# Optimization experiments

Hardware: AMD Instinct MI355X
Metric: run time of the kernel (lower is better)

The kernel has to match this reference:

```python
import jax, jax.numpy as jnp
import numpy as np

B, C, N, H = 8, 256, 2048, 4
DIM = C // H
EPS = 1e-5
SLOPE = 0.2


def conv1x1(W, b, x):
    # W: [out, in], x: [B, in, N] -> [B, out, N]
    return jnp.einsum('oc,bcn->bon', W, x) + b[None, :, None]


def setup_inputs() -> dict:
    key = jax.random.key(0)
    ks = jax.random.split(key, 16)
    s = 1.0 / np.sqrt(C)
    s2 = 1.0 / np.sqrt(2 * C)
    return {
        'init_query': jax.random.normal(ks[0], (B, C, N), jnp.float32),
        'key': jax.random.normal(ks[1], (B, C, N), jnp.float32),
        'value': jax.random.normal(ks[2], (B, C, N), jnp.float32),
        'Wq': jax.random.normal(ks[3], (C, C), jnp.float32) * s,
        'bq': jax.random.normal(ks[4], (C,), jnp.float32) * s,
        'Wk': jax.random.normal(ks[5], (C, C), jnp.float32) * s,
        'bk': jax.random.normal(ks[6], (C,), jnp.float32) * s,
        'Wv': jax.random.normal(ks[7], (C, C), jnp.float32) * s,
        'bv': jax.random.normal(ks[8], (C,), jnp.float32) * s,
        'Wm': jax.random.normal(ks[9], (C, C), jnp.float32) * s,
        'bm': jax.random.normal(ks[10], (C,), jnp.float32) * s,
        'W1': jax.random.normal(ks[11], (2 * C, 2 * C), jnp.float32) * s2,
        'b1': jax.random.normal(ks[12], (2 * C,), jnp.float32) * s2,
        'gamma': jnp.ones((2 * C,), jnp.float32),
        'beta': jnp.zeros((2 * C,), jnp.float32),
        'W2': jax.random.normal(ks[13], (C, 2 * C), jnp.float32) * s2,
        'b2': jnp.zeros((C,), jnp.float32),  # nn.init.constant_(bias, 0.0)
    }


def reference(init_query, key, value, Wq, bq, Wk, bk, Wv, bv, Wm, bm, W1, b1, gamma, beta, W2, b2):
    # projections, then view [B, C, N] -> [B, dim, H, N] (dim outermost, matching torch .view)
    q = conv1x1(Wq, bq, init_query).reshape(B, DIM, H, N)
    k = conv1x1(Wk, bk, key).reshape(B, DIM, H, N)
    v = conv1x1(Wv, bv, value).reshape(B, DIM, H, N)
    scores = jnp.einsum('bdhn,bdhm->bhnm', q, k) / jnp.sqrt(jnp.float32(DIM))
    attn = jax.nn.softmax(scores, axis=-1)  # [B, H, N, N]
    x = jnp.einsum('bhnm,bdhm->bdhn', attn, v).reshape(B, C, N)
    x = conv1x1(Wm, bm, x)
    # post_merge: conv1x1 -> BatchNorm1d (training-mode batch stats) -> LeakyReLU(0.2) -> conv1x1
    h = conv1x1(W1, b1, jnp.concatenate([x, init_query], axis=1))  # [B, 2C, N]
    mu = jnp.mean(h, axis=(0, 2), keepdims=True)
    var = jnp.mean(jnp.square(h - mu), axis=(0, 2), keepdims=True)  # biased var, as torch BN
    hn = (h - mu) / jnp.sqrt(var + EPS) * gamma[None, :, None] + beta[None, :, None]
    hn = jnp.where(hn > 0, hn, SLOPE * hn)
    out = conv1x1(W2, b2, hn)
    return (out, attn)
```

## Files before the change

### kernel.cpp

```cpp
#include <hip/hip_runtime.h>
#include <stdint.h>

typedef __bf16 bf16x8 __attribute__((ext_vector_type(8)));
typedef float f32x4 __attribute__((ext_vector_type(4)));

constexpr int NB = 8;
constexpr int NC = 256;
constexpr int NN = 2048;
constexpr int NH = 4;
constexpr int ND = 64;
constexpr int NC2 = 512;
constexpr size_t TND = (size_t)NB * NN * NC;
__device__ constexpr float C2 = 0.125f * 1.4426950408889634f;

__device__ __forceinline__ ushort f2bf(float f) {
  union { float f; uint32_t u; } x; x.f = f;
  return (ushort)((x.u + 0x7FFFu + ((x.u >> 16) & 1u)) >> 16);
}
__device__ __forceinline__ float bf2f(ushort h) {
  union { uint32_t u; float f; } x; x.u = (uint32_t)h << 16;
  return x.f;
}


__global__ void k_cast(const float* __restrict__ s, ushort* __restrict__ d, int n) {
  int i = blockIdx.x * 256 + threadIdx.x;
  if (i < n) d[i] = f2bf(s[i]);
}

__global__ void k_cast3(const float* __restrict__ s0, const float* __restrict__ s1,
                        const float* __restrict__ s2, ushort* __restrict__ d) {
  int op = blockIdx.y;
  const float* s = op == 0 ? s0 : op == 1 ? s1 : s2;
  int i = blockIdx.x * 256 + threadIdx.x;
  d[(size_t)op * NC * NC + i] = f2bf(s[i]);
}

__global__ void k_cast_wm_perm(const float* __restrict__ s, ushort* __restrict__ d) {
  int i = blockIdx.x * 256 + threadIdx.x;
  int co = i >> 8, j = i & 255;
  int h = j >> 6, dd = j & 63;
  d[i] = f2bf(s[co * NC + dd * NH + h]);
}

__global__ void k_tc3(const float* __restrict__ s0, const float* __restrict__ s1,
                      const float* __restrict__ s2, ushort* __restrict__ d) {
  int n = blockIdx.x * 256 + threadIdx.x;
  int c0 = blockIdx.y * 8;
  int op = blockIdx.z >> 3, b = blockIdx.z & 7;
  const float* s = op == 0 ? s0 : op == 1 ? s1 : s2;
  const float* p = s + ((size_t)b * NC + c0) * NN + n;
  union { ushort u[8]; uint4 v; } t;
#pragma unroll
  for (int i = 0; i < 8; ++i) t.u[i] = f2bf(p[(size_t)i * NN]);
  *(uint4*)(d + (size_t)op * TND + ((size_t)b * NN + n) * NC + c0) = t.v;
}

__global__ void k_ht2(const ushort* __restrict__ s, ushort* __restrict__ d) {
  int n = blockIdx.x * 256 + threadIdx.x;
  int d0 = blockIdx.y * 8;
  int op = blockIdx.z >> 5, zz = blockIdx.z & 31, b = zz >> 2, h = zz & 3;
  const ushort* p = s + (size_t)op * TND + ((size_t)b * NC + (size_t)d0 * NH + h) * NN + n;
  union { ushort u[8]; uint4 v; } t;
#pragma unroll
  for (int i = 0; i < 8; ++i) t.u[i] = p[(size_t)i * NH * NN];
  *(uint4*)(d + (size_t)op * TND + ((size_t)zz * NN + n) * ND + d0) = t.v;
}

__global__ void k_bn_finalize(const float* __restrict__ stats, const float* __restrict__ gamma,
                              const float* __restrict__ beta, float4* __restrict__ aff) {
  int c = blockIdx.x * 256 + threadIdx.x;
  if (c >= NC2) return;
  const float inv_n = 1.f / (float)(NB * NN);
  float mu  = stats[c * 2] * inv_n;
  float var = stats[c * 2 + 1] * inv_n - mu * mu;
  float isg = gamma[c] * rsqrtf(var + 1e-5f);
  aff[c] = make_float4(mu, isg, beta[c], 0.f);
}


__device__ __forceinline__ bf16x8 ldtile(const ushort* base, int lr, int lg, int fc, int ks) {
  int row = fc * 16 + lr;
  int u = (ks * 4 + lg) ^ (lr & 7);
  return *(const bf16x8*)((const char*)base + row * 128 + u * 16);
}

__global__ __launch_bounds__(256, 4) void k_attn(
    const ushort* __restrict__ qt, const ushort* __restrict__ kt,
    const ushort* __restrict__ vnat, float* __restrict__ attn,
    ushort* __restrict__ xT) {
  __shared__ ushort Kl[2][4096];
  __shared__ ushort Vl[2][4096];
  __shared__ ushort Pl[4096];

  const int tid = threadIdx.x;
  const int lane = tid & 63, w = tid >> 6;
  const int lr = lane & 15, lg = lane >> 4;

  int flat = blockIdx.x;
  int xcd = flat & 7, idx = flat >> 3;
  int z = xcd * 4 + (idx >> 5);
  int r0 = (idx & 31) * 64;
  int b = z >> 2, h = z & 3;

  const ushort* kbase = kt + (size_t)z * NN * ND;
  const ushort* vbase = vnat + ((size_t)b * NC + h) * NN;

  const int sr0 = tid >> 3, sc0 = tid & 7;
  const int sr1 = 32 + sr0;
  const int d0 = sr0 * 128 + ((sc0 ^ (sr0 & 7)) << 4);
  const int d1 = sr1 * 128 + ((sc0 ^ (sr1 & 7)) << 4);

  bf16x8 aq0, aq1;
  {
    const ushort* qp = qt + ((size_t)z * NN + r0 + w * 16 + lr) * ND;
    aq0 = *(const bf16x8*)(qp + lg * 8);
    aq1 = *(const bf16x8*)(qp + 32 + lg * 8);
  }

  uint4 gk0, gk1, gv0, gv1;

  gk0 = *(const uint4*)(kbase + (size_t)sr0 * ND + sc0 * 8);
  gk1 = *(const uint4*)(kbase + (size_t)sr1 * ND + sc0 * 8);
  *(uint4*)((char*)Kl[0] + d0) = gk0;
  *(uint4*)((char*)Kl[0] + d1) = gk1;
  __syncthreads();

  float m_ln[4], s_ln[4];
#pragma unroll
  for (int j = 0; j < 4; ++j) { m_ln[j] = -INFINITY; s_ln[j] = 0.f; }

  for (int t = 0; t < 32; ++t) {
    int kb = t & 1;
    if (t < 31) {
      gk0 = *(const uint4*)(kbase + ((size_t)(t + 1) * 64 + sr0) * ND + sc0 * 8);
      gk1 = *(const uint4*)(kbase + ((size_t)(t + 1) * 64 + sr1) * ND + sc0 * 8);
    }
    f32x4 sa[4] = {};
#pragma unroll
    for (int ks = 0; ks < 2; ++ks) {
      bf16x8 aqk = ks ? aq1 : aq0;
#pragma unroll
      for (int fc = 0; fc < 4; ++fc)
        sa[fc] = __builtin_amdgcn_mfma_f32_16x16x32_bf16(aqk, ldtile(Kl[kb], lr, lg, fc, ks), sa[fc], 0, 0, 0);
    }
#pragma unroll
    for (int j = 0; j < 4; ++j) {
      float tm = fmaxf(fmaxf(sa[0][j], sa[1][j]), fmaxf(sa[2][j], sa[3][j]));
      float mn = fmaxf(m_ln[j], tm);
      float es = exp2f((sa[0][j] - mn) * C2) + exp2f((sa[1][j] - mn) * C2)
               + exp2f((sa[2][j] - mn) * C2) + exp2f((sa[3][j] - mn) * C2);
      s_ln[j] = s_ln[j] * exp2f((m_ln[j] - mn) * C2) + es;
      m_ln[j] = mn;
    }
    __syncthreads();
    if (t < 31) {
      *(uint4*)((char*)Kl[kb ^ 1] + d0) = gk0;
      *(uint4*)((char*)Kl[kb ^ 1] + d1) = gk1;
    }
    __syncthreads();
  }

  float m_run[4], inv_s[4];
#pragma unroll
  for (int j = 0; j < 4; ++j) {
    float m = m_ln[j];
#pragma unroll
    for (int o = 1; o < 16; o <<= 1) m = fmaxf(m, __shfl_xor(m, o));
    float c = s_ln[j] * exp2f((m_ln[j] - m) * C2);
#pragma unroll
    for (int o = 1; o < 16; o <<= 1) c += __shfl_xor(c, o);
    m_run[j] = m;
    inv_s[j] = 1.f / c;
  }

  gk0 = *(const uint4*)(kbase + (size_t)sr0 * ND + sc0 * 8);
  gk1 = *(const uint4*)(kbase + (size_t)sr1 * ND + sc0 * 8);
  gv0 = *(const uint4*)(vbase + (size_t)sr0 * 4 * NN + sc0 * 8);
  gv1 = *(const uint4*)(vbase + (size_t)sr1 * 4 * NN + sc0 * 8);
  *(uint4*)((char*)Kl[0] + d0) = gk0;
  *(uint4*)((char*)Kl[0] + d1) = gk1;
  *(uint4*)((char*)Vl[0] + d0) = gv0;
  *(uint4*)((char*)Vl[0] + d1) = gv1;
  __syncthreads();

  f32x4 acc[4] = {};
  const int prow = w * 16 + lr;
  char* plb = (char*)Pl;
  for (int t = 0; t < 32; ++t) {
    int kb = t & 1;
    if (t < 31) {
      gk0 = *(const uint4*)(kbase + ((size_t)(t + 1) * 64 + sr0) * ND + sc0 * 8);
      gk1 = *(const uint4*)(kbase + ((size_t)(t + 1) * 64 + sr1) * ND + sc0 * 8);
      gv0 = *(const uint4*)(vbase + (size_t)sr0 * 4 * NN + (t + 1) * 64 + sc0 * 8);
      gv1 = *(const uint4*)(vbase + (size_t)sr1 * 4 * NN + (t + 1) * 64 + sc0 * 8);
    }
    f32x4 sa[4] = {};
#pragma unroll
    for (int ks = 0; ks < 2; ++ks) {
      bf16x8 aqk = ks ? aq1 : aq0;
#pragma unroll
      for (int fc = 0; fc < 4; ++fc)
        sa[fc] = __builtin_amdgcn_mfma_f32_16x16x32_bf16(aqk, ldtile(Kl[kb], lr, lg, fc, ks), sa[fc], 0, 0, 0);
    }
#pragma unroll
    for (int fc = 0; fc < 4; ++fc)
#pragma unroll
      for (int j = 0; j < 4; ++j) {
        int row = w * 16 + lg * 4 + j;
        float p = exp2f((sa[fc][j] - m_run[j]) * C2) * inv_s[j];
        int byte = (row << 7) + ((fc * 16 + lr) << 1);
        byte ^= (row & 7) << 4;
        *(ushort*)(plb + byte) = f2bf(p);
      }
    float* abase = attn + ((size_t)z * NN + r0) * NN + t * 64;
#pragma unroll
    for (int k = 0; k < 4; ++k) {
      int row = w * 16 + lg + k * 4;
      int byte = (row << 7) + (lr << 3);
      byte ^= (row & 7) << 4;
      const ushort* pq = (const ushort*)(plb + byte);
      f32x4 vv = { bf2f(pq[0]), bf2f(pq[1]), bf2f(pq[2]), bf2f(pq[3]) };
      __builtin_nontemporal_store(vv, (f32x4*)(abase + (size_t)row * NN + lr * 4));
    }
#pragma unroll
    for (int ks = 0; ks < 2; ++ks) {
      int abyte = (prow << 7) + ks * 64 + lg * 16;
      abyte ^= (lr & 7) << 4;
      bf16x8 ap = *(const bf16x8*)(plb + abyte);
#pragma unroll
      for (int fc = 0; fc < 4; ++fc)
        acc[fc] = __builtin_amdgcn_mfma_f32_16x16x32_bf16(ap, ldtile(Vl[kb], lr, lg, fc, ks), acc[fc], 0, 0, 0);
    }
    __syncthreads();
    if (t < 31) {
      *(uint4*)((char*)Kl[kb ^ 1] + d0) = gk0;
      *(uint4*)((char*)Kl[kb ^ 1] + d1) = gk1;
      *(uint4*)((char*)Vl[kb ^ 1] + d0) = gv0;
      *(uint4*)((char*)Vl[kb ^ 1] + d1) = gv1;
    }
    __syncthreads();
  }
#pragma unroll
  for (int fc = 0; fc < 4; ++fc)
#pragma unroll
    for (int j = 0; j < 4; ++j) {
      int n = r0 + w * 16 + lg * 4 + j;
      xT[((size_t)b * NN + n) * NC + h * 64 + fc * 16 + lr] = f2bf(acc[fc][j]);
    }
}


enum GemmMode { M_PROJ = 0, M_WM, M_W1, M_W2 };

template <int MODE>
__global__ __launch_bounds__(256) void k_gemm(
    const ushort* __restrict__ A, const ushort* __restrict__ A2,
    const ushort* __restrict__ Bm,
    const float* __restrict__ bias, const float* __restrict__ bias_k,
    const float* __restrict__ bias_v, const float4* __restrict__ aff,
    float* __restrict__ stats, float* __restrict__ outf, ushort* __restrict__ outb) {
  constexpr int BR = (MODE == M_WM || MODE == M_W2) ? 64 : 128;
  constexpr int BC = 128;
  constexpr int KT = (MODE == M_PROJ || MODE == M_WM) ? 256 : 512;
  constexpr int FR = BR / 32;
  constexpr int FC = 4;
  constexpr int LDL = 72;

  __shared__ ushort ldsA[BR * LDL];
  __shared__ ushort ldsB[BC * LDL];

  const int tid = threadIdx.x;
  const int lane = tid & 63, wave = tid >> 6;
  const int wr = (wave >> 1) * (FR * 16), wc = (wave & 1) * (FC * 16);
  const int lr = lane & 15, lk = (lane >> 4) * 8;
  const int c0 = blockIdx.x * BC, r0 = blockIdx.y * BR;
  const int op = (MODE == M_PROJ) ? (int)(blockIdx.z >> 3) : 0;
  const size_t z = (MODE == M_PROJ) ? (blockIdx.z & 7) : blockIdx.z;

  f32x4 acc[FR][FC] = {};

  for (int kk = 0; kk < KT; kk += 64) {
    {
      const ushort* src; int ld;
      if constexpr (MODE == M_PROJ)        { src = A + (size_t)op * NC * NC + (size_t)r0 * NC + kk; ld = NC; }
      else if constexpr (MODE == M_WM)     { src = A + (z * NN + r0) * (size_t)NC + kk; ld = NC; }
      else if constexpr (MODE == M_W1) {
        if (kk < NC) src = A  + (z * NN + r0) * (size_t)NC + kk;
        else         src = A2 + (z * NN + r0) * (size_t)NC + (kk - NC);
        ld = NC;
      } else { src = A + (size_t)r0 * NC2 + kk; ld = NC2; }
#pragma unroll
      for (int i = 0; i < BR / 32; ++i) {
        int off = (tid + i * 256) * 8, row = off >> 6, k = off & 63;
        *(uint4*)&ldsA[row * LDL + k] = *(const uint4*)(src + (size_t)row * ld + k);
      }
    }
    if constexpr (MODE == M_W2) {
      const ushort* src = Bm + (z * NN + c0) * (size_t)NC2 + kk;
#pragma unroll
      for (int i = 0; i < BC / 32; ++i) {
        int off = (tid + i * 256) * 8, row = off >> 6, k = off & 63;
        union { ushort u[8]; uint4 v; } t, o;
        t.v = *(const uint4*)(src + (size_t)row * NC2 + k);
#pragma unroll
        for (int e = 0; e < 8; ++e) {
          float4 pr = aff[kk + k + e];
          float y = (bf2f(t.u[e]) - pr.x) * pr.y + pr.z;
          y = y > 0.f ? y : 0.2f * y;
          o.u[e] = f2bf(y);
        }
        *(uint4*)&ldsB[row * LDL + k] = o.v;
      }
    } else {
      const ushort* src; int ld;
      if constexpr (MODE == M_PROJ)        { src = Bm + (size_t)op * TND + (z * NN + c0) * (size_t)NC + kk; ld = NC; }
      else if constexpr (MODE == M_WM)     { src = Bm + (size_t)c0 * NC + kk; ld = NC; }
      else                                  { src = Bm + (size_t)c0 * NC2 + kk; ld = NC2; }
#pragma unroll
      for (int i = 0; i < BC / 32; ++i) {
        int off = (tid + i * 256) * 8, row = off >> 6, k = off & 63;
        *(uint4*)&ldsB[row * LDL + k] = *(const uint4*)(src + (size_t)row * ld + k);
      }
    }
    __syncthreads();
#pragma unroll
    for (int ks = 0; ks < 2; ++ks) {
      bf16x8 afr[FR], bfr[FC];
#pragma unroll
      for (int fr = 0; fr < FR; ++fr)
        afr[fr] = *(const bf16x8*)&ldsA[(wr + fr * 16 + lr) * LDL + ks * 32 + lk];
#pragma unroll
      for (int fc = 0; fc < FC; ++fc)
        bfr[fc] = *(const bf16x8*)&ldsB[(wc + fc * 16 + lr) * LDL + ks * 32 + lk];
#pragma unroll
      for (int fr = 0; fr < FR; ++fr)
#pragma unroll
        for (int fc = 0; fc < FC; ++fc)
          acc[fr][fc] = __builtin_amdgcn_mfma_f32_16x16x32_bf16(afr[fr], bfr[fc], acc[fr][fc], 0, 0, 0);
    }
    __syncthreads();
  }

  float sfc[FC], qfc[FC];
#pragma unroll
  for (int fc = 0; fc < FC; ++fc) { sfc[fc] = 0.f; qfc[fc] = 0.f; }
#pragma unroll
  for (int fr = 0; fr < FR; ++fr)
#pragma unroll
    for (int fc = 0; fc < FC; ++fc)
#pragma unroll
      for (int j = 0; j < 4; ++j) {
        int r = r0 + wr + fr * 16 + (lane >> 4) * 4 + j;
        int c = c0 + wc + fc * 16 + lr;
        float v = acc[fr][fc][j];
        if constexpr (MODE == M_PROJ) {
          const float* bb = op == 0 ? bias : op == 1 ? bias_k : bias_v;
          v += bb[r];
          outb[(size_t)op * TND + (z * NC + r) * (size_t)NN + c] = f2bf(v);
        } else if constexpr (MODE == M_WM) {
          v += bias[c];
          outb[(z * NN + r) * (size_t)NC + c] = f2bf(v);
        } else if constexpr (MODE == M_W1) {
          v += bias[c];
          outb[(z * NN + r) * (size_t)NC2 + c] = f2bf(v);
          sfc[fc] += v; qfc[fc] += v * v;
        } else {
          v += bias[r];
          outf[(z * NC + r) * (size_t)NN + c] = v;
        }
      }
  if constexpr (MODE == M_W1) {
#pragma unroll
    for (int fc = 0; fc < FC; ++fc) {
      float s1 = sfc[fc], s2 = qfc[fc];
      s1 += __shfl_xor(s1, 16); s1 += __shfl_xor(s1, 32);
      s2 += __shfl_xor(s2, 16); s2 += __shfl_xor(s2, 32);
      if (lane < 16) {
        int ch = c0 + wc + fc * 16 + lane;
        atomicAdd(&stats[ch * 2],     s1);
        atomicAdd(&stats[ch * 2 + 1], s2);
      }
    }
  }
}


extern "C" void kernel_launch(void* const* d_in, const int* in_sizes, int n_in,
                              void* d_out, int out_size, void* d_ws, size_t ws_size,
                              hipStream_t stream) {
  const float* iq    = (const float*)d_in[0];
  const float* keyi  = (const float*)d_in[1];
  const float* vali  = (const float*)d_in[2];
  const float* Wq = (const float*)d_in[3];  const float* bq = (const float*)d_in[4];
  const float* Wk = (const float*)d_in[5];  const float* bk = (const float*)d_in[6];
  const float* Wv = (const float*)d_in[7];  const float* bv = (const float*)d_in[8];
  const float* Wm = (const float*)d_in[9];  const float* bm = (const float*)d_in[10];
  const float* W1 = (const float*)d_in[11]; const float* b1 = (const float*)d_in[12];
  const float* gamma = (const float*)d_in[13]; const float* beta = (const float*)d_in[14];
  const float* W2 = (const float*)d_in[15]; const float* b2 = (const float*)d_in[16];

  float* out  = (float*)d_out;
  float* attn = out + (size_t)NB * NC * NN;

  uint8_t* cur = (uint8_t*)d_ws;
  auto alloc = [&](size_t bytes) { uint8_t* p = cur; cur += (bytes + 255) & ~(size_t)255; return p; };
  ushort* wq_b = (ushort*)alloc((size_t)NC * NC * 2 * 3);
  ushort* wm_b = (ushort*)alloc((size_t)NC * NC * 2);
  ushort* w1_b = (ushort*)alloc((size_t)NC2 * NC2 * 2);
  ushort* w2_b = (ushort*)alloc((size_t)NC * NC2 * 2);
  ushort* iqT   = (ushort*)alloc(TND * 2 * 3);
  ushort* q_nat = (ushort*)alloc(TND * 2 * 3);
  ushort* qt    = (ushort*)alloc(TND * 2 * 2);
  ushort* xT    = (ushort*)alloc(TND * 2);
  ushort* xmT   = (ushort*)alloc(TND * 2);
  ushort* hT    = (ushort*)alloc((size_t)NB * NN * NC2 * 2);
  float*  stats = (float*)alloc(NC2 * 2 * 4);
  float4* aff   = (float4*)alloc(NC2 * 16);
  ushort* kT    = iqT + TND;
  ushort* vT    = iqT + 2 * TND;
  ushort* v_nat = q_nat + 2 * TND;
  ushort* kt    = qt + TND;

  hipMemsetAsync(stats, 0, NC2 * 2 * 4, stream);

  k_cast3<<<dim3(256, 3), 256, 0, stream>>>(Wq, Wk, Wv, wq_b);
  k_cast_wm_perm<<<dim3(256), 256, 0, stream>>>(Wm, wm_b);
  k_cast<<<dim3(1024), 256, 0, stream>>>(W1, w1_b, NC2 * NC2);
  k_cast<<<dim3(512), 256, 0, stream>>>(W2, w2_b, NC * NC2);

  k_tc3<<<dim3(8, 32, 24), 256, 0, stream>>>(iq, keyi, vali, iqT);

  k_gemm<M_PROJ><<<dim3(16, 2, 24), 256, 0, stream>>>(wq_b, nullptr, iqT, bq, bk, bv, nullptr, nullptr, nullptr, q_nat);

  k_ht2<<<dim3(8, 8, 64), 256, 0, stream>>>(q_nat, qt);

  k_attn<<<dim3(1024), 256, 0, stream>>>(qt, kt, v_nat, attn, xT);

  k_gemm<M_WM><<<dim3(2, 32, 8), 256, 0, stream>>>(xT, nullptr, wm_b, bm, nullptr, nullptr, nullptr, nullptr, nullptr, xmT);

  k_gemm<M_W1><<<dim3(4, 16, 8), 256, 0, stream>>>(xmT, iqT, w1_b, b1, nullptr, nullptr, nullptr, stats, nullptr, hT);

  k_bn_finalize<<<dim3(2), 256, 0, stream>>>(stats, gamma, beta, aff);

  k_gemm<M_W2><<<dim3(16, 4, 8), 256, 0, stream>>>(w2_b, nullptr, hT, b2, nullptr, nullptr, aff, nullptr, out, nullptr);
}
```

Before: 290.6 us.

## Fuse input transpose-casts and head transpose into projection GEMM; pipeline attention loads

Removes the standalone fp32-to-bf16 transpose kernel and the head-transpose kernel. The projection GEMM now stages fp32 inputs directly into LDS and writes Q/K in per-head layout through an LDS transpose, with Wq/Wk rows permuted at cast time. The W1 GEMM reads init_query fp32 directly. Attention now prefetches K/V two tiles ahead, which drops one barrier per iteration. It also folds the softmax normalization into the exponent via log2 of the sum and stores fp32 probabilities straight to attn. These changes cut intermediate HBM traffic and kernel launches, at the cost of more complex GEMM staging and uncoalesced scalar attn stores.

After: 320.0 us. 1.1x slower.

```diff
diff --git a/kernel.cpp b/kernel.cpp
--- a/kernel.cpp
+++ b/kernel.cpp
@@ -28,12 +28,14 @@
   if (i < n) d[i] = f2bf(s[i]);
 }
 
-__global__ void k_cast3(const float* __restrict__ s0, const float* __restrict__ s1,
-                        const float* __restrict__ s2, ushort* __restrict__ d) {
+__global__ void k_cast_qkv(const float* __restrict__ s0, const float* __restrict__ s1,
+                           const float* __restrict__ s2, ushort* __restrict__ d) {
   int op = blockIdx.y;
   const float* s = op == 0 ? s0 : op == 1 ? s1 : s2;
   int i = blockIdx.x * 256 + threadIdx.x;
-  d[(size_t)op * NC * NC + i] = f2bf(s[i]);
+  int r = i >> 8, c = i & 255;
+  int orig = op < 2 ? (((r & 63) << 2) | (r >> 6)) : r;
+  d[(size_t)op * NC * NC + i] = f2bf(s[orig * NC + c]);
 }
 
 __global__ void k_cast_wm_perm(const float* __restrict__ s, ushort* __restrict__ d) {
@@ -41,30 +43,6 @@
   int co = i >> 8, j = i & 255;
   int h = j >> 6, dd = j & 63;
   d[i] = f2bf(s[co * NC + dd * NH + h]);
-}
-
-__global__ void k_tc3(const float* __restrict__ s0, const float* __restrict__ s1,
-                      const float* __restrict__ s2, ushort* __restrict__ d) {
-  int n = blockIdx.x * 256 + threadIdx.x;
-  int c0 = blockIdx.y * 8;
-  int op = blockIdx.z >> 3, b = blockIdx.z & 7;
-  const float* s = op == 0 ? s0 : op == 1 ? s1 : s2;
-  const float* p = s + ((size_t)b * NC + c0) * NN + n;
-  union { ushort u[8]; uint4 v; } t;
-#pragma unroll
-  for (int i = 0; i < 8; ++i) t.u[i] = f2bf(p[(size_t)i * NN]);
-  *(uint4*)(d + (size_t)op * TND + ((size_t)b * NN + n) * NC + c0) = t.v;
-}
-
-__global__ void k_ht2(const ushort* __restrict__ s, ushort* __restrict__ d) {
-  int n = blockIdx.x * 256 + threadIdx.x;
-  int d0 = blockIdx.y * 8;
-  int op = blockIdx.z >> 5, zz = blockIdx.z & 31, b = zz >> 2, h = zz & 3;
-  const ushort* p = s + (size_t)op * TND + ((size_t)b * NC + (size_t)d0 * NH + h) * NN + n;
-  union { ushort u[8]; uint4 v; } t;
-#pragma unroll
-  for (int i = 0; i < 8; ++i) t.u[i] = p[(size_t)i * NH * NN];
-  *(uint4*)(d + (size_t)op * TND + ((size_t)zz * NN + n) * ND + d0) = t.v;
 }
 
 __global__ void k_bn_finalize(const float* __restrict__ stats, const float* __restrict__ gamma,
@@ -124,6 +102,8 @@
   gk1 = *(const uint4*)(kbase + (size_t)sr1 * ND + sc0 * 8);
   *(uint4*)((char*)Kl[0] + d0) = gk0;
   *(uint4*)((char*)Kl[0] + d1) = gk1;
+  gk0 = *(const uint4*)(kbase + (size_t)(64 + sr0) * ND + sc0 * 8);
+  gk1 = *(const uint4*)(kbase + (size_t)(64 + sr1) * ND + sc0 * 8);
   __syncthreads();
 
   float m_ln[4], s_ln[4];
@@ -133,8 +113,12 @@
   for (int t = 0; t < 32; ++t) {
     int kb = t & 1;
     if (t < 31) {
-      gk0 = *(const uint4*)(kbase + ((size_t)(t + 1) * 64 + sr0) * ND + sc0 * 8);
-      gk1 = *(const uint4*)(kbase + ((size_t)(t + 1) * 64 + sr1) * ND + sc0 * 8);
+      *(uint4*)((char*)Kl[kb ^ 1] + d0) = gk0;
+      *(uint4*)((char*)Kl[kb ^ 1] + d1) = gk1;
+    }
+    if (t < 30) {
+      gk0 = *(const uint4*)(kbase + ((size_t)(t + 2) * 64 + sr0) * ND + sc0 * 8);
+      gk1 = *(const uint4*)(kbase + ((size_t)(t + 2) * 64 + sr1) * ND + sc0 * 8);
     }
     f32x4 sa[4] = {};
 #pragma unroll
@@ -148,20 +132,16 @@
     for (int j = 0; j < 4; ++j) {
       float tm = fmaxf(fmaxf(sa[0][j], sa[1][j]), fmaxf(sa[2][j], sa[3][j]));
       float mn = fmaxf(m_ln[j], tm);
-      float es = exp2f((sa[0][j] - mn) * C2) + exp2f((sa[1][j] - mn) * C2)
-               + exp2f((sa[2][j] - mn) * C2) + exp2f((sa[3][j] - mn) * C2);
-      s_ln[j] = s_ln[j] * exp2f((m_ln[j] - mn) * C2) + es;
+      float mnC = mn * C2;
+      float es = exp2f(fmaf(sa[0][j], C2, -mnC)) + exp2f(fmaf(sa[1][j], C2, -mnC))
+               + exp2f(fmaf(sa[2][j], C2, -mnC)) + exp2f(fmaf(sa[3][j], C2, -mnC));
+      s_ln[j] = s_ln[j] * exp2f(fmaf(m_ln[j], C2, -mnC)) + es;
       m_ln[j] = mn;
     }
     __syncthreads();
-    if (t < 31) {
-      *(uint4*)((char*)Kl[kb ^ 1] + d0) = gk0;
-      *(uint4*)((char*)Kl[kb ^ 1] + d1) = gk1;
-    }
-    __syncthreads();
-  }
-
-  float m_run[4], inv_s[4];
+  }
+
+  float mC[4];
 #pragma unroll
   for (int j = 0; j < 4; ++j) {
     float m = m_ln[j];
@@ -170,8 +150,7 @@
     float c = s_ln[j] * exp2f((m_ln[j] - m) * C2);
 #pragma unroll
     for (int o = 1; o < 16; o <<= 1) c += __shfl_xor(c, o);
-    m_run[j] = m;
-    inv_s[j] = 1.f / c;
+    mC[j] = m * C2 + __log2f(c);
   }
 
   gk0 = *(const uint4*)(kbase + (size_t)sr0 * ND + sc0 * 8);
@@ -182,6 +161,10 @@
   *(uint4*)((char*)Kl[0] + d1) = gk1;
   *(uint4*)((char*)Vl[0] + d0) = gv0;
   *(uint4*)((char*)Vl[0] + d1) = gv1;
+  gk0 = *(const uint4*)(kbase + (size_t)(64 + sr0) * ND + sc0 * 8);
+  gk1 = *(const uint4*)(kbase + (size_t)(64 + sr1) * ND + sc0 * 8);
+  gv0 = *(const uint4*)(vbase + (size_t)sr0 * 4 * NN + 64 + sc0 * 8);
+  gv1 = *(const uint4*)(vbase + (size_t)sr1 * 4 * NN + 64 + sc0 * 8);
   __syncthreads();
 
   f32x4 acc[4] = {};
@@ -190,55 +173,46 @@
   for (int t = 0; t < 32; ++t) {
     int kb = t & 1;
     if (t < 31) {
-      gk0 = *(const uint4*)(kbase + ((size_t)(t + 1) * 64 + sr0) * ND + sc0 * 8);
-      gk1 = *(const uint4*)(kbase + ((size_t)(t + 1) * 64 + sr1) * ND + sc0 * 8);
-      gv0 = *(const uint4*)(vbase + (size_t)sr0 * 4 * NN + (t + 1) * 64 + sc0 * 8);
-      gv1 = *(const uint4*)(vbase + (size_t)sr1 * 4 * NN + (t + 1) * 64 + sc0 * 8);
-    }
-    f32x4 sa[4] = {};
-#pragma unroll
-    for (int ks = 0; ks < 2; ++ks) {
-      bf16x8 aqk = ks ? aq1 : aq0;
-#pragma unroll
-      for (int fc = 0; fc < 4; ++fc)
-        sa[fc] = __builtin_amdgcn_mfma_f32_16x16x32_bf16(aqk, ldtile(Kl[kb], lr, lg, fc, ks), sa[fc], 0, 0, 0);
-    }
-#pragma unroll
-    for (int fc = 0; fc < 4; ++fc)
-#pragma unroll
-      for (int j = 0; j < 4; ++j) {
-        int row = w * 16 + lg * 4 + j;
-        float p = exp2f((sa[fc][j] - m_run[j]) * C2) * inv_s[j];
-        int byte = (row << 7) + ((fc * 16 + lr) << 1);
-        byte ^= (row & 7) << 4;
-        *(ushort*)(plb + byte) = f2bf(p);
-      }
-    float* abase = attn + ((size_t)z * NN + r0) * NN + t * 64;
-#pragma unroll
-    for (int k = 0; k < 4; ++k) {
-      int row = w * 16 + lg + k * 4;
-      int byte = (row << 7) + (lr << 3);
-      byte ^= (row & 7) << 4;
-      const ushort* pq = (const ushort*)(plb + byte);
-      f32x4 vv = { bf2f(pq[0]), bf2f(pq[1]), bf2f(pq[2]), bf2f(pq[3]) };
-      __builtin_nontemporal_store(vv, (f32x4*)(abase + (size_t)row * NN + lr * 4));
-    }
-#pragma unroll
-    for (int ks = 0; ks < 2; ++ks) {
-      int abyte = (prow << 7) + ks * 64 + lg * 16;
-      abyte ^= (lr & 7) << 4;
-      bf16x8 ap = *(const bf16x8*)(plb + abyte);
-#pragma unroll
-      for (int fc = 0; fc < 4; ++fc)
-        acc[fc] = __builtin_amdgcn_mfma_f32_16x16x32_bf16(ap, ldtile(Vl[kb], lr, lg, fc, ks), acc[fc], 0, 0, 0);
-    }
-    __syncthreads();
-    if (t < 31) {
       *(uint4*)((char*)Kl[kb ^ 1] + d0) = gk0;
       *(uint4*)((char*)Kl[kb ^ 1] + d1) = gk1;
       *(uint4*)((char*)Vl[kb ^ 1] + d0) = gv0;
       *(uint4*)((char*)Vl[kb ^ 1] + d1) = gv1;
     }
+    if (t < 30) {
+      gk0 = *(const uint4*)(kbase + ((size_t)(t + 2) * 64 + sr0) * ND + sc0 * 8);
+      gk1 = *(const uint4*)(kbase + ((size_t)(t + 2) * 64 + sr1) * ND + sc0 * 8);
+      gv0 = *(const uint4*)(vbase + (size_t)sr0 * 4 * NN + (t + 2) * 64 + sc0 * 8);
+      gv1 = *(const uint4*)(vbase + (size_t)sr1 * 4 * NN + (t + 2) * 64 + sc0 * 8);
+    }
+    f32x4 sa[4] = {};
+#pragma unroll
+    for (int ks = 0; ks < 2; ++ks) {
+      bf16x8 aqk = ks ? aq1 : aq0;
+#pragma unroll
+      for (int fc = 0; fc < 4; ++fc)
+        sa[fc] = __builtin_amdgcn_mfma_f32_16x16x32_bf16(aqk, ldtile(Kl[kb], lr, lg, fc, ks), sa[fc], 0, 0, 0);
+    }
+    float* abase = attn + ((size_t)z * NN + r0) * NN + t * 64;
+#pragma unroll
+    for (int fc = 0; fc < 4; ++fc)
+#pragma unroll
+      for (int j = 0; j < 4; ++j) {
+        int row = w * 16 + lg * 4 + j;
+        float p = exp2f(fmaf(sa[fc][j], C2, -mC[j]));
+        __builtin_nontemporal_store(p, abase + (size_t)row * NN + fc * 16 + lr);
+        int byte = (row << 7) + ((fc * 16 + lr) << 1);
+        byte ^= (row & 7) << 4;
+        *(ushort*)(plb + byte) = f2bf(p);
+      }
+#pragma unroll
+    for (int ks = 0; ks < 2; ++ks) {
+      int abyte = (prow << 7) + ks * 64 + lg * 16;
+      abyte ^= (prow & 7) << 4;
+      bf16x8 ap = *(const bf16x8*)(plb + abyte);
+#pragma unroll
+      for (int fc = 0; fc < 4; ++fc)
+        acc[fc] = __builtin_amdgcn_mfma_f32_16x16x32_bf16(ap, ldtile(Vl[kb], lr, lg, fc, ks), acc[fc], 0, 0, 0);
+    }
     __syncthreads();
   }
 #pragma unroll
@@ -255,11 +229,11 @@
 
 template <int MODE>
 __global__ __launch_bounds__(256) void k_gemm(
-    const ushort* __restrict__ A, const ushort* __restrict__ A2,
-    const ushort* __restrict__ Bm,
-    const float* __restrict__ bias, const float* __restrict__ bias_k,
-    const float* __restrict__ bias_v, const float4* __restrict__ aff,
-    float* __restrict__ stats, float* __restrict__ outf, ushort* __restrict__ outb) {
+    const ushort* __restrict__ A, const ushort* __restrict__ Bm,
+    const float* __restrict__ Fa, const float* __restrict__ Fb, const float* __restrict__ Fc,
+    const float* __restrict__ b0, const float* __restrict__ b1v, const float* __restrict__ b2v,
+    const float4* __restrict__ aff, float* __restrict__ stats,
+    float* __restrict__ outf, ushort* __restrict__ outb, ushort* __restrict__ outb2) {
   constexpr int BR = (MODE == M_WM || MODE == M_W2) ? 64 : 128;
   constexpr int BC = 128;
   constexpr int KT = (MODE == M_PROJ || MODE == M_WM) ? 256 : 512;
@@ -267,36 +241,60 @@
   constexpr int FC = 4;
   constexpr int LDL = 72;
 
-  __shared__ ushort ldsA[BR * LDL];
-  __shared__ ushort ldsB[BC * LDL];
+  __shared__ ushort ldsU[BR * LDL + BC * LDL];
+  ushort* ldsA = ldsU;
+  ushort* ldsB = ldsU + BR * LDL;
 
   const int tid = threadIdx.x;
   const int lane = tid & 63, wave = tid >> 6;
   const int wr = (wave >> 1) * (FR * 16), wc = (wave & 1) * (FC * 16);
-  const int lr = lane & 15, lk = (lane >> 4) * 8;
+  const int lr = lane & 15, lg = lane >> 4, lk = lg * 8;
   const int c0 = blockIdx.x * BC, r0 = blockIdx.y * BR;
   const int op = (MODE == M_PROJ) ? (int)(blockIdx.z >> 3) : 0;
   const size_t z = (MODE == M_PROJ) ? (blockIdx.z & 7) : blockIdx.z;
 
+  auto stage_t = [&](ushort* dst, const float* src) {
+    int n = tid & 127, half = tid >> 7;
+#pragma unroll
+    for (int u = 0; u < 4; ++u) {
+      int cg = half + u * 2;
+      union { ushort us[8]; uint4 v; } pk;
+#pragma unroll
+      for (int e = 0; e < 8; ++e)
+        pk.us[e] = f2bf(src[(size_t)(cg * 8 + e) * NN + n]);
+      *(uint4*)&dst[n * LDL + cg * 8] = pk.v;
+    }
+  };
+
   f32x4 acc[FR][FC] = {};
 
   for (int kk = 0; kk < KT; kk += 64) {
-    {
+    if constexpr (MODE == M_W1) {
+      if (kk < NC) {
+        const ushort* src = A + (z * NN + r0) * (size_t)NC + kk;
+#pragma unroll
+        for (int i = 0; i < BR / 32; ++i) {
+          int off = (tid + i * 256) * 8, row = off >> 6, k = off & 63;
+          *(uint4*)&ldsA[row * LDL + k] = *(const uint4*)(src + (size_t)row * NC + k);
+        }
+      } else {
+        stage_t(ldsA, Fa + ((size_t)z * NC + (kk - NC)) * NN + r0);
+      }
+    } else {
       const ushort* src; int ld;
       if constexpr (MODE == M_PROJ)        { src = A + (size_t)op * NC * NC + (size_t)r0 * NC + kk; ld = NC; }
       else if constexpr (MODE == M_WM)     { src = A + (z * NN + r0) * (size_t)NC + kk; ld = NC; }
-      else if constexpr (MODE == M_W1) {
-        if (kk < NC) src = A  + (z * NN + r0) * (size_t)NC + kk;
-        else         src = A2 + (z * NN + r0) * (size_t)NC + (kk - NC);
-        ld = NC;
-      } else { src = A + (size_t)r0 * NC2 + kk; ld = NC2; }
+      else                                  { src = A + (size_t)r0 * NC2 + kk; ld = NC2; }
 #pragma unroll
       for (int i = 0; i < BR / 32; ++i) {
         int off = (tid + i * 256) * 8, row = off >> 6, k = off & 63;
         *(uint4*)&ldsA[row * LDL + k] = *(const uint4*)(src + (size_t)row * ld + k);
       }
     }
-    if constexpr (MODE == M_W2) {
+    if constexpr (MODE == M_PROJ) {
+      const float* Fsel = op == 0 ? Fa : op == 1 ? Fb : Fc;
+      stage_t(ldsB, Fsel + ((size_t)z * NC + kk) * NN + c0);
+    } else if constexpr (MODE == M_W2) {
       const ushort* src = Bm + (z * NN + c0) * (size_t)NC2 + kk;
 #pragma unroll
       for (int i = 0; i < BC / 32; ++i) {
@@ -314,8 +312,7 @@
       }
     } else {
       const ushort* src; int ld;
-      if constexpr (MODE == M_PROJ)        { src = Bm + (size_t)op * TND + (z * NN + c0) * (size_t)NC + kk; ld = NC; }
-      else if constexpr (MODE == M_WM)     { src = Bm + (size_t)c0 * NC + kk; ld = NC; }
+      if constexpr (MODE == M_WM)          { src = Bm + (size_t)c0 * NC + kk; ld = NC; }
       else                                  { src = Bm + (size_t)c0 * NC2 + kk; ld = NC2; }
 #pragma unroll
       for (int i = 0; i < BC / 32; ++i) {
@@ -342,6 +339,56 @@
     __syncthreads();
   }
 
+  if constexpr (MODE == M_PROJ) {
+    if (op < 2) {
+      const float* bb = op == 0 ? b0 : b1v;
+      char* tb = (char*)ldsU;
+#pragma unroll
+      for (int fr = 0; fr < FR; ++fr)
+#pragma unroll
+        for (int fc = 0; fc < FC; ++fc) {
+          int n_l = wc + fc * 16 + lr;
+          int rb = wr + fr * 16 + lg * 4;
+          union { ushort u[4]; uint2 v; } pk;
+#pragma unroll
+          for (int j = 0; j < 4; ++j) {
+            int r = r0 + rb + j;
+            pk.u[j] = f2bf(acc[fr][fc][j] + bb[((r & 63) << 2) | (r >> 6)]);
+          }
+          int byte = n_l * 256 + rb * 2;
+          byte ^= (n_l & 7) << 4;
+          *(uint2*)(tb + byte) = pk.v;
+        }
+      __syncthreads();
+      ushort* dst = outb + (size_t)op * TND;
+#pragma unroll
+      for (int hh = 0; hh < 2; ++hh) {
+        size_t zz = z * 4 + (r0 >> 6) + hh;
+#pragma unroll
+        for (int u = 0; u < 4; ++u) {
+          int seg = u * 256 + tid;
+          int n_l = seg >> 3, dd = (seg & 7) * 8;
+          int byte = n_l * 256 + (hh * 64 + dd) * 2;
+          byte ^= (n_l & 7) << 4;
+          uint4 v = *(const uint4*)(tb + byte);
+          *(uint4*)(dst + (zz * NN + c0 + n_l) * (size_t)ND + dd) = v;
+        }
+      }
+    } else {
+#pragma unroll
+      for (int fr = 0; fr < FR; ++fr)
+#pragma unroll
+        for (int fc = 0; fc < FC; ++fc)
+#pragma unroll
+          for (int j = 0; j < 4; ++j) {
+            int r = r0 + wr + fr * 16 + lg * 4 + j;
+            int c = c0 + wc + fc * 16 + lr;
+            outb2[(z * NC + r) * (size_t)NN + c] = f2bf(acc[fr][fc][j] + b2v[r]);
+          }
+    }
+    return;
+  }
+
   float sfc[FC], qfc[FC];
 #pragma unroll
   for (int fc = 0; fc < FC; ++fc) { sfc[fc] = 0.f; qfc[fc] = 0.f; }
@@ -351,22 +398,18 @@
     for (int fc = 0; fc < FC; ++fc)
 #pragma unroll
       for (int j = 0; j < 4; ++j) {
-        int r = r0 + wr + fr * 16 + (lane >> 4) * 4 + j;
+        int r = r0 + wr + fr * 16 + lg * 4 + j;
         int c = c0 + wc + fc * 16 + lr;
         float v = acc[fr][fc][j];
-        if constexpr (MODE == M_PROJ) {
-          const float* bb = op == 0 ? bias : op == 1 ? bias_k : bias_v;
-          v += bb[r];
-          outb[(size_t)op * TND + (z * NC + r) * (size_t)NN + c] = f2bf(v);
-        } else if constexpr (MODE == M_WM) {
-          v += bias[c];
+        if constexpr (MODE == M_WM) {
+          v += b0[c];
           outb[(z * NN + r) * (size_t)NC + c] = f2bf(v);
         } else if constexpr (MODE == M_W1) {
-          v += bias[c];
+          v += b0[c];
           outb[(z * NN + r) * (size_t)NC2 + c] = f2bf(v);
           sfc[fc] += v; qfc[fc] += v * v;
         } else {
-          v += bias[r];
+          v += b0[r];
           outf[(z * NC + r) * (size_t)NN + c] = v;
         }
       }
@@ -405,43 +448,39 @@
 
   uint8_t* cur = (uint8_t*)d_ws;
   auto alloc = [&](size_t bytes) { uint8_t* p = cur; cur += (bytes + 255) & ~(size_t)255; return p; };
-  ushort* wq_b = (ushort*)alloc((size_t)NC * NC * 2 * 3);
-  ushort* wm_b = (ushort*)alloc((size_t)NC * NC * 2);
-  ushort* w1_b = (ushort*)alloc((size_t)NC2 * NC2 * 2);
-  ushort* w2_b = (ushort*)alloc((size_t)NC * NC2 * 2);
-  ushort* iqT   = (ushort*)alloc(TND * 2 * 3);
-  ushort* q_nat = (ushort*)alloc(TND * 2 * 3);
-  ushort* qt    = (ushort*)alloc(TND * 2 * 2);
+  ushort* wqkv  = (ushort*)alloc((size_t)NC * NC * 2 * 3);
+  ushort* wm_b  = (ushort*)alloc((size_t)NC * NC * 2);
+  ushort* w1_b  = (ushort*)alloc((size_t)NC2 * NC2 * 2);
+  ushort* w2_b  = (ushort*)alloc((size_t)NC * NC2 * 2);
+  ushort* qtkt  = (ushort*)alloc(TND * 2 * 2);
+  ushort* v_nat = (ushort*)alloc(TND * 2);
   ushort* xT    = (ushort*)alloc(TND * 2);
   ushort* xmT   = (ushort*)alloc(TND * 2);
   ushort* hT    = (ushort*)alloc((size_t)NB * NN * NC2 * 2);
   float*  stats = (float*)alloc(NC2 * 2 * 4);
   float4* aff   = (float4*)alloc(NC2 * 16);
-  ushort* kT    = iqT + TND;
-  ushort* vT    = iqT + 2 * TND;
-  ushort* v_nat = q_nat + 2 * TND;
-  ushort* kt    = qt + TND;
-
-  hipMemsetAsync(stats, 0, NC2 * 2 * 4, stream);
-
-  k_cast3<<<dim3(256, 3), 256, 0, stream>>>(Wq, Wk, Wv, wq_b);
+  ushort* kt    = qtkt + TND;
+
+  (void)hipMemsetAsync(stats, 0, NC2 * 2 * 4, stream);
+
+  k_cast_qkv<<<dim3(256, 3), 256, 0, stream>>>(Wq, Wk, Wv, wqkv);
   k_cast_wm_perm<<<dim3(256), 256, 0, stream>>>(Wm, wm_b);
   k_cast<<<dim3(1024), 256, 0, stream>>>(W1, w1_b, NC2 * NC2);
   k_cast<<<dim3(512), 256, 0, stream>>>(W2, w2_b, NC * NC2);
 
-  k_tc3<<<dim3(8, 32, 24), 256, 0, stream>>>(iq, keyi, vali, iqT);
-
-  k_gemm<M_PROJ><<<dim3(16, 2, 24), 256, 0, stream>>>(wq_b, nullptr, iqT, bq, bk, bv, nullptr, nullptr, nullptr, q_nat);
-
-  k_ht2<<<dim3(8, 8, 64), 256, 0, stream>>>(q_nat, qt);
-
-  k_attn<<<dim3(1024), 256, 0, stream>>>(qt, kt, v_nat, attn, xT);
-
-  k_gemm<M_WM><<<dim3(2, 32, 8), 256, 0, stream>>>(xT, nullptr, wm_b, bm, nullptr, nullptr, nullptr, nullptr, nullptr, xmT);
-
-  k_gemm<M_W1><<<dim3(4, 16, 8), 256, 0, stream>>>(xmT, iqT, w1_b, b1, nullptr, nullptr, nullptr, stats, nullptr, hT);
+  k_gemm<M_PROJ><<<dim3(16, 2, 24), 256, 0, stream>>>(
+      wqkv, nullptr, iq, keyi, vali, bq, bk, bv, nullptr, nullptr, nullptr, qtkt, v_nat);
+
+  k_attn<<<dim3(1024), 256, 0, stream>>>(qtkt, kt, v_nat, attn, xT);
+
+  k_gemm<M_WM><<<dim3(2, 32, 8), 256, 0, stream>>>(
+      xT, wm_b, nullptr, nullptr, nullptr, bm, nullptr, nullptr, nullptr, nullptr, nullptr, xmT, nullptr);
+
+  k_gemm<M_W1><<<dim3(4, 16, 8), 256, 0, stream>>>(
+      xmT, w1_b, iq, nullptr, nullptr, b1, nullptr, nullptr, nullptr, stats, nullptr, hT, nullptr);
 
   k_bn_finalize<<<dim3(2), 256, 0, stream>>>(stats, gamma, beta, aff);
 
-  k_gemm<M_W2><<<dim3(16, 4, 8), 256, 0, stream>>>(w2_b, nullptr, hT, b2, nullptr, nullptr, aff, nullptr, out, nullptr);
-}
+  k_gemm<M_W2><<<dim3(16, 4, 8), 256, 0, stream>>>(
+      w2_b, hT, nullptr, nullptr, nullptr, b2, nullptr, nullptr, aff, nullptr, out, nullptr, nullptr);
+}
```
